# Optimization experiments

Measured on AMD Instinct MI355X. Metric: run time of the kernel, lower is better.

The kernel has to match this reference:

```python
import jax, jax.numpy as jnp
import numpy as np

N = 384      # max_nodes
H = 256      # layers[0] == layers[1] == layers[2]
Z = 128      # dim_z
ED = 128     # edge_dim
AH = ED // 2 # attention hidden

# complete directed graph: combinations (i<j) then reversed pairs
_i, _j = np.triu_indices(N, k=1)
_SRC = jnp.asarray(np.concatenate([_i, _j]), dtype=jnp.int32)  # edge_index[0]
_DST = jnp.asarray(np.concatenate([_j, _i]), dtype=jnp.int32)  # edge_index[1]


def setup_inputs() -> dict:
    key = jax.random.key(0)
    ks = jax.random.split(key, 16)
    def p(k, shape, fan_in):
        return jax.random.normal(k, shape, dtype=jnp.float32) * (1.0 / np.sqrt(fan_in))
    return {
        "z": jax.random.normal(ks[0], (1, Z), dtype=jnp.float32),
        # GRU (torch layout: W_ih [3H, Z], W_hh [3H, H]; gate order r, z, n)
        "gru_Wih": p(ks[1], (3 * H, Z), Z),
        "gru_Whh": p(ks[2], (3 * H, H), H),
        "gru_bih": jnp.zeros((3 * H,), jnp.float32),
        "gru_bhh": jnp.zeros((3 * H,), jnp.float32),
        # edge_generator MLP: 2H -> 4H -> ED
        "eg_W1": p(ks[3], (2 * H, 4 * H), 2 * H), "eg_b1": jnp.zeros((4 * H,), jnp.float32),
        "eg_W2": p(ks[4], (4 * H, ED), 4 * H),   "eg_b2": jnp.zeros((ED,), jnp.float32),
        # attention MLPs: (ED+H) -> ED//2 -> 1
        "att0_W1": p(ks[5], (ED + H, AH), ED + H), "att0_b1": jnp.zeros((AH,), jnp.float32),
        "att0_W2": p(ks[6], (AH, 1), AH),           "att0_b2": jnp.zeros((1,), jnp.float32),
        "att1_W1": p(ks[7], (ED + H, AH), ED + H), "att1_b1": jnp.zeros((AH,), jnp.float32),
        "att1_W2": p(ks[8], (AH, 1), AH),           "att1_b2": jnp.zeros((1,), jnp.float32),
        # EdgeConv output linears: H -> H
        "conv0_W": p(ks[9], (H, H), H),  "conv0_b": jnp.zeros((H,), jnp.float32),
        "conv1_W": p(ks[10], (H, H), H), "conv1_b": jnp.zeros((H,), jnp.float32),
    }


def _forward(z, gru_Wih, gru_Whh, gru_bih, gru_bhh,
             eg_W1, eg_b1, eg_W2, eg_b2,
             att0_W1, att0_b1, att0_W2, att0_b2,
             att1_W1, att1_b1, att1_W2, att1_b2,
             conv0_W, conv0_b, conv1_W, conv1_b):
    # --- GRU node generation: input is the same latent z at every step ---
    gi = z[0] @ gru_Wih.T + gru_bih            # [3H], constant per step
    gir, giz, gin = jnp.split(gi, 3)
    def step(h, _):
        gh = h @ gru_Whh.T + gru_bhh
        ghr, ghz, ghn = jnp.split(gh, 3)
        r = jax.nn.sigmoid(gir + ghr)
        u = jax.nn.sigmoid(giz + ghz)
        n = jnp.tanh(gin + r * ghn)
        h2 = (1.0 - u) * n + u * h
        return h2, h2
    _, nodes = jax.lax.scan(step, jnp.zeros((H,), z.dtype), None, length=N)  # [N, H]

    # --- edge features over the complete directed graph ---
    pairs = jnp.concatenate([nodes[_SRC], nodes[_DST]], axis=-1)            # [E, 2H]
    edges = jax.nn.relu(pairs @ eg_W1 + eg_b1) @ eg_W2 + eg_b2              # [E, ED]

    # --- EdgeConv: gather src, attention MLP gate, scatter-sum, linear ---
    def conv(x, aW1, ab1, aW2, ab2, W, b):
        xs = x[_SRC]                                                        # [E, H]
        a_in = jnp.concatenate([edges, xs], axis=-1)                        # [E, ED+H]
        att = jax.nn.sigmoid(jax.nn.relu(a_in @ aW1 + ab1) @ aW2 + ab2)     # [E, 1]
        agg = jax.ops.segment_sum(att * xs, _DST, num_segments=N)           # [N, H]
        return agg @ W + b

    x = jax.nn.relu(conv(nodes, att0_W1, att0_b1, att0_W2, att0_b2, conv0_W, conv0_b))
    x = conv(x, att1_W1, att1_b1, att1_W2, att1_b2, conv1_W, conv1_b)
    return jnp.sum(x, axis=0)                                               # [H]


def reference(z, gru_Wih, gru_Whh, gru_bih, gru_bhh,
              eg_W1, eg_b1, eg_W2, eg_b2,
              att0_W1, att0_b1, att0_W2, att0_b2,
              att1_W1, att1_b1, att1_W2, att1_b2,
              conv0_W, conv0_b, conv1_W, conv1_b):
    return _forward(z, gru_Wih, gru_Whh, gru_bih, gru_bhh,
                    eg_W1, eg_b1, eg_W2, eg_b2,
                    att0_W1, att0_b1, att0_W2, att0_b2,
                    att1_W1, att1_b1, att1_W2, att1_b2,
                    conv0_W, conv0_b, conv1_W, conv1_b)
```

## Files before the change

### kernel.cpp

```cpp
#include <hip/hip_runtime.h>
#include <hip/hip_fp16.h>
#include <cstdint>

#define DEV static __device__ __forceinline__

typedef _Float16 h2v __attribute__((ext_vector_type(2)));
typedef _Float16 half8 __attribute__((ext_vector_type(8)));
typedef float float4v __attribute__((ext_vector_type(4)));

union U32H2 { uint32_t u; _Float16 f[2]; };

DEV uint32_t pack_f2(float a, float b) {
    auto p = __builtin_amdgcn_cvt_pkrtz(a, b);
    return __builtin_bit_cast(uint32_t, p);
}

DEV half8 bc8(uint4 v) { return __builtin_bit_cast(half8, v); }

DEV float sigmoidf_(float x) { return 1.0f / (1.0f + __expf(-x)); }

DEV void gl_lds16(const void* gsrc, void* ldst) {
    __builtin_amdgcn_global_load_lds(
        (const __attribute__((address_space(1))) uint32_t*)gsrc,
        (__attribute__((address_space(3))) uint32_t*)ldst, 16, 0, 0);
}

DEV float pick4(float4v lo, float4v hi, int bsel, int r) {
    float v0 = bsel ? hi[0] : lo[0];
    float v1 = bsel ? hi[1] : lo[1];
    float v2 = bsel ? hi[2] : lo[2];
    float v3 = bsel ? hi[3] : lo[3];
    float x01 = (r & 1) ? v1 : v0;
    float x23 = (r & 1) ? v3 : v2;
    return (r & 2) ? x23 : x01;
}

static const size_t OFF_W16T  = 0;
static const size_t OFF_GI    = 98304;
static const size_t OFF_CC    = 99072;
static const size_t OFF_BF    = 99200;
static const size_t OFF_NODES = 164736;
static const size_t OFF_PF    = 263040;
static const size_t OFF_QF    = 459648;
static const size_t OFF_R0    = 656256;
static const size_t OFF_R1    = 680832;
static const size_t OFF_TT    = 705408;
static const size_t OFF_ATT0  = 10142592;
static const size_t OFF_ATT1  = 10290048;
static const size_t OFF_AGG   = 10437504;
static const size_t OFF_X0    = 10535808;
static const size_t OFF_CS    = 10634112;
static const size_t OFF_V     = 10634496;
static const size_t WS_TOTAL  = 10634752;

__global__ void k_prep_w16(const float* __restrict__ Whh, uint32_t* __restrict__ WL) {
    int o4 = blockIdx.x * 256 + threadIdx.x;
    int c = o4 >> 9, t = o4 & 511;
    int rt = c >> 3, kt = c & 7;
    int lane = t & 63, wv = t >> 6;
    int row = (rt >> 1) * 256 + wv * 32 + ((rt & 1) << 4) + (lane & 15);
    int k0 = kt*32 + (lane >> 4)*8;
    const float* src = Whh + row*256 + k0;
    uint4 o;
    o.x = pack_f2(src[0], src[1]);
    o.y = pack_f2(src[2], src[3]);
    o.z = pack_f2(src[4], src[5]);
    o.w = pack_f2(src[6], src[7]);
    ((uint4*)WL)[o4] = o;
}

__global__ void k_prep_gi(const float* __restrict__ z, const float* __restrict__ Wih,
                          const float* __restrict__ bih, const float* __restrict__ bhh,
                          float* __restrict__ gs) {
    int o = blockIdx.x * 256 + threadIdx.x;
    float acc = bih[o];
    if (o < 512) acc += bhh[o];
    for (int i = 0; i < 128; ++i) acc += Wih[o*128 + i] * z[i];
    gs[o] = acc;
}

__global__ void k_prep_cc(const float* __restrict__ eg_b2, const float* __restrict__ a0W1,
                          const float* __restrict__ a1W1, float* __restrict__ cc) {
    int t = threadIdx.x;
    const float* A = (t < 64) ? a0W1 : a1W1;
    int j = t & 63;
    float acc = 0.f;
    for (int i = 0; i < 128; ++i) acc += eg_b2[i] * A[i*64 + j];
    cc[t] = acc;
}

__global__ void k_prep_w2a(const float* __restrict__ eg_W2, const float* __restrict__ a0W1,
                           const float* __restrict__ a1W1, uint32_t* __restrict__ BF) {
    int idx = blockIdx.x * 256 + threadIdx.x;
    int k2 = idx >> 7, n = idx & 127;
    const float* A = (n < 64) ? (a0W1 + n) : (a1W1 + (n - 64));
    const float* w0 = eg_W2 + (2*k2) * 128;
    float a = 0.f, b = 0.f;
    for (int i = 0; i < 128; ++i) {
        float av = A[i*64];
        a += w0[i] * av;
        b += w0[128 + i] * av;
    }
    int kk = k2 >> 4, jgrp = (k2 >> 2) & 3, sub = k2 & 3;
    int lane = jgrp*16 + (n & 15), t = n >> 4;
    BF[((kk*8 + t)*64 + lane)*4 + sub] = pack_f2(a, b);
}

__global__ void __launch_bounds__(512, 2)
k_gru(const float* __restrict__ gs, const float* __restrict__ bhh,
      const uint32_t* __restrict__ WL, float* __restrict__ nodes) {
    int tid = threadIdx.x;
    int lane = tid & 63, wv = tid >> 6;
    int kq = lane >> 4, c = lane & 15;
    __shared__ __align__(16) _Float16 hh16[512];

    uint4 w[48];
    const uint4* wl4 = (const uint4*)WL;
    #pragma unroll
    for (int cc = 0; cc < 48; ++cc) w[cc] = wl4[cc*512 + tid];
    #pragma unroll
    for (int cc = 0; cc < 48; ++cc)
        asm volatile("" : "+a"(w[cc].x), "+a"(w[cc].y), "+a"(w[cc].z), "+a"(w[cc].w));

    const float L2E = 1.44269504088896f;
    int r = c & 3, bsel = (c >> 2) & 1;
    int i_loc = kq*4 + r + bsel*16;
    int gidx = wv*32 + i_loc;
    float pr = -L2E * gs[gidx];
    float pz = -L2E * gs[256 + gidx];
    float gin_l = gs[512 + gidx];
    float bn_l  = bhh[512 + gidx];
    float pn = -2.f * L2E * gin_l;
    bool active = (c < 8);

    float h = 0.f;
    if (tid < 256) ((uint32_t*)hh16)[tid] = 0u;
    __syncthreads();

    const float4v z4 = {0.f, 0.f, 0.f, 0.f};
    int par = 0;
    for (int t = 0; t < 384; ++t) {
        const _Float16* hb = hh16 + par*256 + kq*8;
        uint4 b[8];
        #pragma unroll
        for (int kt = 0; kt < 8; ++kt) b[kt] = *(const uint4*)(hb + kt*32);

        float4v d[6];
        #pragma unroll
        for (int rt = 0; rt < 6; ++rt)
            d[rt] = __builtin_amdgcn_mfma_f32_16x16x32_f16(bc8(w[rt*8]), bc8(b[0]), z4, 0, 0, 0);
        #pragma unroll
        for (int kt = 1; kt < 8; ++kt)
            #pragma unroll
            for (int rt = 0; rt < 6; ++rt)
                d[rt] = __builtin_amdgcn_mfma_f32_16x16x32_f16(bc8(w[rt*8 + kt]), bc8(b[kt]), d[rt], 0, 0, 0);

        float ghr = pick4(d[0], d[1], bsel, r);
        float ghz = pick4(d[2], d[3], bsel, r);
        float ghn = pick4(d[4], d[5], bsel, r);

        float er = __builtin_amdgcn_exp2f(__builtin_fmaf(ghr, -L2E, pr));
        float rg = __builtin_amdgcn_rcpf(1.f + er);
        float eu = __builtin_amdgcn_exp2f(__builtin_fmaf(ghz, -L2E, pz));
        float u  = __builtin_amdgcn_rcpf(1.f + eu);
        float tm = ghn + bn_l;
        float q  = __builtin_fmaf(rg * tm, -2.f * L2E, pn);
        float e2 = __builtin_amdgcn_exp2f(q);
        float nn = __builtin_fmaf(2.f, __builtin_amdgcn_rcpf(1.f + e2), -1.f);
        h = nn + u * (h - nn);

        if (active) {
            hh16[(par ^ 1)*256 + gidx] = (_Float16)h;
            nodes[t*256 + gidx] = h;
        }
        asm volatile("s_waitcnt lgkmcnt(0)" ::: "memory");
        __builtin_amdgcn_sched_barrier(0);
        __builtin_amdgcn_s_barrier();
        __builtin_amdgcn_sched_barrier(0);
        par ^= 1;
    }
}

__global__ void k_pq(const float* __restrict__ nodes, const float* __restrict__ eg_W1,
                     const float* __restrict__ eg_b1, const float* __restrict__ a0W1,
                     const float* __restrict__ a0b1, const float* __restrict__ cc,
                     uint32_t* __restrict__ PF, uint32_t* __restrict__ QF,
                     float* __restrict__ R0) {
    int tid = threadIdx.x;
    int s0 = blockIdx.x * 4;
    __shared__ float ns[4][256];
    #pragma unroll
    for (int q = 0; q < 4; ++q) ns[q][tid] = nodes[(s0+q)*256 + tid];
    __syncthreads();

    int k0 = tid * 4;
    float acc[4][4];
    #pragma unroll
    for (int q = 0; q < 4; ++q) { acc[q][0]=0;acc[q][1]=0;acc[q][2]=0;acc[q][3]=0; }
    for (int i = 0; i < 256; ++i) {
        float4 wv = *(const float4*)&eg_W1[i*1024 + k0];
        #pragma unroll
        for (int q = 0; q < 4; ++q) {
            float nv = ns[q][i];
            acc[q][0] += nv*wv.x; acc[q][1] += nv*wv.y;
            acc[q][2] += nv*wv.z; acc[q][3] += nv*wv.w;
        }
    }
    float4 bv = *(const float4*)&eg_b1[k0];
    {
        int kk = k0 >> 5;
        int lgrp = ((k0 >> 3) & 3) * 16;
        int sub = (k0 & 7) >> 1;
        #pragma unroll
        for (int q = 0; q < 4; ++q) {
            int s = s0 + q, g = s >> 4, srow = s & 15;
            uint2 pw;
            pw.x = pack_f2(acc[q][0] + bv.x, acc[q][1] + bv.y);
            pw.y = pack_f2(acc[q][2] + bv.z, acc[q][3] + bv.w);
            *(uint2*)(PF + (((g*32 + kk)*64 + lgrp + srow) << 2) + sub) = pw;
        }
    }

    #pragma unroll
    for (int q = 0; q < 4; ++q) { acc[q][0]=0;acc[q][1]=0;acc[q][2]=0;acc[q][3]=0; }
    for (int i = 0; i < 256; ++i) {
        float4 wv = *(const float4*)&eg_W1[(256+i)*1024 + k0];
        #pragma unroll
        for (int q = 0; q < 4; ++q) {
            float nv = ns[q][i];
            acc[q][0] += nv*wv.x; acc[q][1] += nv*wv.y;
            acc[q][2] += nv*wv.z; acc[q][3] += nv*wv.w;
        }
    }
    #pragma unroll
    for (int q = 0; q < 4; ++q) {
        uint2 pw;
        pw.x = pack_f2(acc[q][0], acc[q][1]);
        pw.y = pack_f2(acc[q][2], acc[q][3]);
        ((uint2*)QF)[(s0+q)*256 + tid] = pw;
    }

    int srow = tid >> 6, j = tid & 63;
    float racc = a0b1[j] + cc[j];
    for (int i = 0; i < 256; ++i) racc += ns[srow][i] * a0W1[(128+i)*64 + j];
    R0[(s0+srow)*64 + j] = racc;
}

__global__ void __launch_bounds__(256, 2)
k_phaseA_mfma(const uint32_t* __restrict__ PF, const uint32_t* __restrict__ QF,
              const uint32_t* __restrict__ BF, uint32_t* __restrict__ TT) {
    __shared__ __align__(16) char smem[69632];
    uint4* Qs4 = (uint4*)smem;
    uint4* Ps4 = (uint4*)(smem + 32768);
    uint4* Bs4 = (uint4*)(smem + 36864);

    int tid = threadIdx.x;
    int lane = tid & 63, wv = tid >> 6;
    int g = blockIdx.x, d0 = blockIdx.y * 16;

    {
        const char* src = (const char*)(QF + (size_t)d0 * 512);
        for (int off = wv*1024 + lane*16; off < 32768; off += 4096)
            gl_lds16(src + off, (char*)Qs4 + off);
    }

    float4v acc[4][8];
    #pragma unroll
    for (int t = 0; t < 4; ++t)
        #pragma unroll
        for (int n = 0; n < 8; ++n) acc[t][n] = 0.f;

    for (int c = 0; c < 8; ++c) {
        __syncthreads();
        {
            const char* psrc = (const char*)(PF + (size_t)(g*32 + c*4) * 256);
            for (int off = wv*1024 + lane*16; off < 4096; off += 4096)
                gl_lds16(psrc + off, (char*)Ps4 + off);
            const char* bsrc = (const char*)(BF + (size_t)c * 8192);
            for (int off = wv*1024 + lane*16; off < 32768; off += 4096)
                gl_lds16(bsrc + off, (char*)Bs4 + off);
        }
        __syncthreads();

        #pragma unroll
        for (int kkl = 0; kkl < 4; ++kkl) {
            int kkg = c*4 + kkl;
            half8 b[8];
            #pragma unroll
            for (int n = 0; n < 8; ++n) b[n] = bc8(Bs4[(kkl*8 + n)*64 + lane]);
            half8 p8 = bc8(Ps4[kkl*64 + lane]);
            #pragma unroll
            for (int t = 0; t < 4; ++t) {
                half8 q8 = bc8(Qs4[(wv*4 + t)*128 + kkg*4 + (lane >> 4)]);
                half8 x = p8 + q8;
                half8 z = 0;
                x = __builtin_elementwise_max(x, z);
                #pragma unroll
                for (int n = 0; n < 8; ++n)
                    acc[t][n] = __builtin_amdgcn_mfma_f32_16x16x32_f16(x, b[n], acc[t][n], 0, 0, 0);
            }
        }
    }

    _Float16* epi = (_Float16*)(smem + 36864);
    int cn = lane & 15, rhi = (lane >> 4) * 4;
    for (int half = 0; half < 2; ++half) {
        __syncthreads();
        #pragma unroll
        for (int t = 0; t < 4; ++t) {
            int dl = wv*4 + t;
            #pragma unroll
            for (int n = 0; n < 4; ++n) {
                int j = n*16 + cn;
                float4v v = acc[t][half*4 + n];
                #pragma unroll
                for (int r = 0; r < 4; ++r)
                    epi[((rhi + r)*16 + dl)*64 + j] = (_Float16)v[r];
            }
        }
        __syncthreads();
        int srow = tid >> 4, dl = tid & 15;
        const uint4* src = (const uint4*)(epi + tid*64);
        uint4* dst = (uint4*)(TT + ((size_t)((g*16 + srow)*384 + d0 + dl))*64 + half*32);
        #pragma unroll
        for (int q = 0; q < 8; ++q) dst[q] = src[q];
    }
}

__global__ void k_att(const uint32_t* __restrict__ TT, const float* __restrict__ R,
                      const float* __restrict__ w2, const float* __restrict__ b2,
                      int off, float* __restrict__ ATT) {
    int p = blockIdx.x * 256 + threadIdx.x;
    int s = p / 384, d = p - s * 384;
    __shared__ float w2s[64];
    if (threadIdx.x < 64) w2s[threadIdx.x] = w2[threadIdx.x];
    __syncthreads();
    const uint4* tp = (const uint4*)(TT + (size_t)p*64 + off);
    const float* rp = R + s*64;
    float logit = b2[0];
    #pragma unroll
    for (int m = 0; m < 8; ++m) {
        uint4 tv = tp[m];
        uint32_t us[4] = {tv.x, tv.y, tv.z, tv.w};
        #pragma unroll
        for (int q = 0; q < 4; ++q) {
            U32H2 c; c.u = us[q];
            int j = m*8 + q*2;
            float h0 = fmaxf((float)c.f[0] + rp[j],   0.f);
            float h1 = fmaxf((float)c.f[1] + rp[j+1], 0.f);
            logit += h0*w2s[j] + h1*w2s[j+1];
        }
    }
    float a = 1.f / (1.f + __expf(-logit));
    ATT[p] = (s == d) ? 0.f : a;
}

__global__ void __launch_bounds__(256)
k_agg(const float* __restrict__ ATT, const float* __restrict__ X,
      float* __restrict__ AGG) {
    int tid = threadIdx.x;
    int d0 = blockIdx.x * 16;
    __shared__ float att_s[16][17];
    float acc[16];
    #pragma unroll
    for (int dl = 0; dl < 16; ++dl) acc[dl] = 0.f;

    for (int s0 = 0; s0 < 384; s0 += 16) {
        __syncthreads();
        {
            int row = tid >> 4, col = tid & 15;
            att_s[row][col] = ATT[(s0 + row)*384 + d0 + col];
        }
        __syncthreads();
        #pragma unroll 4
        for (int ss = 0; ss < 16; ++ss) {
            float x = X[(s0 + ss)*256 + tid];
            #pragma unroll
            for (int dl = 0; dl < 16; ++dl) acc[dl] += att_s[ss][dl] * x;
        }
    }
    #pragma unroll
    for (int dl = 0; dl < 16; ++dl)
        AGG[(d0 + dl)*256 + tid] = acc[dl];
}

__global__ void k_x0r1(const float* __restrict__ AGG, const float* __restrict__ W,
                       const float* __restrict__ b, const float* __restrict__ a1W1,
                       const float* __restrict__ a1b1, const float* __restrict__ cc,
                       float* __restrict__ X0, float* __restrict__ R1) {
    int d = blockIdx.x, tid = threadIdx.x;
    __shared__ float ag[256];
    __shared__ float xs[256];
    ag[tid] = AGG[d*256 + tid];
    __syncthreads();
    float acc = b[tid];
    for (int i = 0; i < 256; ++i) acc += ag[i] * W[i*256 + tid];
    acc = fmaxf(acc, 0.f);
    X0[d*256 + tid] = acc;
    xs[tid] = acc;
    __syncthreads();
    if (tid < 64) {
        float r = a1b1[tid] + cc[64 + tid];
        for (int i = 0; i < 256; ++i) r += xs[i] * a1W1[(128+i)*64 + tid];
        R1[d*64 + tid] = r;
    }
}

__global__ void k_colsum(const float* __restrict__ ATT, float* __restrict__ CS) {
    int s = blockIdx.x, t = threadIdx.x;
    float acc = 0.f;
    for (int d = t; d < 384; d += 64) acc += ATT[s*384 + d];
    for (int o = 32; o > 0; o >>= 1) acc += __shfl_down(acc, o, 64);
    if (t == 0) CS[s] = acc;
}

__global__ void k_v(const float* __restrict__ CS, const float* __restrict__ X0,
                    float* __restrict__ V) {
    int tid = threadIdx.x;
    __shared__ float cs[384];
    for (int q = tid; q < 384; q += 256) cs[q] = CS[q];
    __syncthreads();
    float acc = 0.f;
    for (int s = 0; s < 384; s += 4) {
        acc += cs[s]*X0[s*256 + tid] + cs[s+1]*X0[(s+1)*256 + tid]
             + cs[s+2]*X0[(s+2)*256 + tid] + cs[s+3]*X0[(s+3)*256 + tid];
    }
    V[tid] = acc;
}

__global__ void k_out(const float* __restrict__ V, const float* __restrict__ W,
                      const float* __restrict__ b, float* __restrict__ out) {
    int tid = threadIdx.x;
    __shared__ float vs[256];
    vs[tid] = V[tid];
    __syncthreads();
    float acc = 384.f * b[tid];
    for (int i = 0; i < 256; ++i) acc += vs[i] * W[i*256 + tid];
    out[tid] = acc;
}

extern "C" void kernel_launch(void* const* d_in, const int* in_sizes, int n_in,
                              void* d_out, int out_size, void* d_ws, size_t ws_size,
                              hipStream_t stream) {
    if (ws_size < WS_TOTAL * sizeof(uint32_t)) return;

    const float* z    = (const float*)d_in[0];
    const float* Wih  = (const float*)d_in[1];
    const float* Whh  = (const float*)d_in[2];
    const float* bih  = (const float*)d_in[3];
    const float* bhh  = (const float*)d_in[4];
    const float* egW1 = (const float*)d_in[5];
    const float* egb1 = (const float*)d_in[6];
    const float* egW2 = (const float*)d_in[7];
    const float* egb2 = (const float*)d_in[8];
    const float* a0W1 = (const float*)d_in[9];
    const float* a0b1 = (const float*)d_in[10];
    const float* a0W2 = (const float*)d_in[11];
    const float* a0b2 = (const float*)d_in[12];
    const float* a1W1 = (const float*)d_in[13];
    const float* a1b1 = (const float*)d_in[14];
    const float* a1W2 = (const float*)d_in[15];
    const float* a1b2 = (const float*)d_in[16];
    const float* c0W  = (const float*)d_in[17];
    const float* c0b  = (const float*)d_in[18];
    const float* c1W  = (const float*)d_in[19];
    const float* c1b  = (const float*)d_in[20];

    uint32_t* ws   = (uint32_t*)d_ws;
    uint32_t* WL   = ws + OFF_W16T;
    float*    gi   = (float*)(ws + OFF_GI);
    float*    cc   = (float*)(ws + OFF_CC);
    uint32_t* BF   = ws + OFF_BF;
    float*    nodes= (float*)(ws + OFF_NODES);
    uint32_t* PF   = ws + OFF_PF;
    uint32_t* QF   = ws + OFF_QF;
    float*    R0   = (float*)(ws + OFF_R0);
    float*    R1   = (float*)(ws + OFF_R1);
    uint32_t* TT   = ws + OFF_TT;
    float*    ATT0 = (float*)(ws + OFF_ATT0);
    float*    ATT1 = (float*)(ws + OFF_ATT1);
    float*    AGG  = (float*)(ws + OFF_AGG);
    float*    X0   = (float*)(ws + OFF_X0);
    float*    CS   = (float*)(ws + OFF_CS);
    float*    V    = (float*)(ws + OFF_V);
    float*    out  = (float*)d_out;

    hipLaunchKernelGGL(k_prep_w16,    dim3(96),  dim3(256), 0, stream, Whh, WL);
    hipLaunchKernelGGL(k_prep_gi,     dim3(3),   dim3(256), 0, stream, z, Wih, bih, bhh, gi);
    hipLaunchKernelGGL(k_prep_cc,     dim3(1),   dim3(128), 0, stream, egb2, a0W1, a1W1, cc);
    hipLaunchKernelGGL(k_prep_w2a,    dim3(256), dim3(256), 0, stream, egW2, a0W1, a1W1, BF);
    hipLaunchKernelGGL(k_gru,         dim3(1),   dim3(512), 0, stream, gi, bhh, WL, nodes);
    hipLaunchKernelGGL(k_pq,          dim3(96),  dim3(256), 0, stream, nodes, egW1, egb1, a0W1, a0b1, cc, PF, QF, R0);
    hipLaunchKernelGGL(k_phaseA_mfma, dim3(24, 24), dim3(256), 0, stream, PF, QF, BF, TT);
    hipLaunchKernelGGL(k_att,         dim3(576), dim3(256), 0, stream, TT, R0, a0W2, a0b2, 0,  ATT0);
    hipLaunchKernelGGL(k_agg,         dim3(24),  dim3(256), 0, stream, ATT0, nodes, AGG);
    hipLaunchKernelGGL(k_x0r1,        dim3(384), dim3(256), 0, stream, AGG, c0W, c0b, a1W1, a1b1, cc, X0, R1);
    hipLaunchKernelGGL(k_att,         dim3(576), dim3(256), 0, stream, TT, R1, a1W2, a1b2, 32, ATT1);
    hipLaunchKernelGGL(k_colsum,      dim3(384), dim3(64),  0, stream, ATT1, CS);
    hipLaunchKernelGGL(k_v,           dim3(1),   dim3(256), 0, stream, CS, X0, V);
    hipLaunchKernelGGL(k_out,         dim3(1),   dim3(256), 0, stream, V, c1W, c1b, out);
}
```

Measured before the change: 704.8 us.

## Merge prep kernels, double-buffer phase-A staging, fuse colsum/out, reorder GRU gates

The four weight-prep kernels become one launch, and the colsum, v and out kernels fold into an atomic column sum inside the second attention kernel plus a single k_vout kernel. Phase A now double-buffers the P/B tiles in half-chunks so the next tile loads while the current one is multiplied. The GRU step computes the reset-gate MFMAs first so its sigmoid can overlap the remaining gate MFMAs, and k_att caches the R rows in shared memory. The goal is fewer launches and less exposed latency; the atomics add a memset and make the float summation order nondeterministic.

```diff
diff --git a/kernel.cpp b/kernel.cpp
--- a/kernel.cpp
+++ b/kernel.cpp
@@ -53,57 +53,58 @@
 static const size_t OFF_V     = 10634496;
 static const size_t WS_TOTAL  = 10634752;
 
-__global__ void k_prep_w16(const float* __restrict__ Whh, uint32_t* __restrict__ WL) {
-    int o4 = blockIdx.x * 256 + threadIdx.x;
-    int c = o4 >> 9, t = o4 & 511;
-    int rt = c >> 3, kt = c & 7;
-    int lane = t & 63, wv = t >> 6;
-    int row = (rt >> 1) * 256 + wv * 32 + ((rt & 1) << 4) + (lane & 15);
-    int k0 = kt*32 + (lane >> 4)*8;
-    const float* src = Whh + row*256 + k0;
-    uint4 o;
-    o.x = pack_f2(src[0], src[1]);
-    o.y = pack_f2(src[2], src[3]);
-    o.z = pack_f2(src[4], src[5]);
-    o.w = pack_f2(src[6], src[7]);
-    ((uint4*)WL)[o4] = o;
-}
-
-__global__ void k_prep_gi(const float* __restrict__ z, const float* __restrict__ Wih,
-                          const float* __restrict__ bih, const float* __restrict__ bhh,
-                          float* __restrict__ gs) {
-    int o = blockIdx.x * 256 + threadIdx.x;
-    float acc = bih[o];
-    if (o < 512) acc += bhh[o];
-    for (int i = 0; i < 128; ++i) acc += Wih[o*128 + i] * z[i];
-    gs[o] = acc;
-}
-
-__global__ void k_prep_cc(const float* __restrict__ eg_b2, const float* __restrict__ a0W1,
-                          const float* __restrict__ a1W1, float* __restrict__ cc) {
-    int t = threadIdx.x;
-    const float* A = (t < 64) ? a0W1 : a1W1;
-    int j = t & 63;
-    float acc = 0.f;
-    for (int i = 0; i < 128; ++i) acc += eg_b2[i] * A[i*64 + j];
-    cc[t] = acc;
-}
-
-__global__ void k_prep_w2a(const float* __restrict__ eg_W2, const float* __restrict__ a0W1,
-                           const float* __restrict__ a1W1, uint32_t* __restrict__ BF) {
-    int idx = blockIdx.x * 256 + threadIdx.x;
-    int k2 = idx >> 7, n = idx & 127;
-    const float* A = (n < 64) ? (a0W1 + n) : (a1W1 + (n - 64));
-    const float* w0 = eg_W2 + (2*k2) * 128;
-    float a = 0.f, b = 0.f;
-    for (int i = 0; i < 128; ++i) {
-        float av = A[i*64];
-        a += w0[i] * av;
-        b += w0[128 + i] * av;
-    }
-    int kk = k2 >> 4, jgrp = (k2 >> 2) & 3, sub = k2 & 3;
-    int lane = jgrp*16 + (n & 15), t = n >> 4;
-    BF[((kk*8 + t)*64 + lane)*4 + sub] = pack_f2(a, b);
+__global__ void k_prep_all(const float* __restrict__ Whh, uint32_t* __restrict__ WL,
+                           const float* __restrict__ z, const float* __restrict__ Wih,
+                           const float* __restrict__ bih, const float* __restrict__ bhh,
+                           float* __restrict__ gs,
+                           const float* __restrict__ egb2, const float* __restrict__ a0W1,
+                           const float* __restrict__ a1W1, float* __restrict__ cc,
+                           const float* __restrict__ egW2, uint32_t* __restrict__ BF) {
+    int bb = blockIdx.x;
+    if (bb < 96) {
+        int o4 = bb * 256 + threadIdx.x;
+        int c = o4 >> 9, t = o4 & 511;
+        int rt = c >> 3, kt = c & 7;
+        int lane = t & 63, wv = t >> 6;
+        int row = (rt >> 1) * 256 + wv * 32 + ((rt & 1) << 4) + (lane & 15);
+        int k0 = kt*32 + (lane >> 4)*8;
+        const float* src = Whh + row*256 + k0;
+        uint4 o;
+        o.x = pack_f2(src[0], src[1]);
+        o.y = pack_f2(src[2], src[3]);
+        o.z = pack_f2(src[4], src[5]);
+        o.w = pack_f2(src[6], src[7]);
+        ((uint4*)WL)[o4] = o;
+    } else if (bb < 99) {
+        int o = (bb - 96) * 256 + threadIdx.x;
+        float acc = bih[o];
+        if (o < 512) acc += bhh[o];
+        for (int i = 0; i < 128; ++i) acc += Wih[o*128 + i] * z[i];
+        gs[o] = acc;
+    } else if (bb == 99) {
+        int t = threadIdx.x;
+        if (t < 128) {
+            const float* A = (t < 64) ? a0W1 : a1W1;
+            int j = t & 63;
+            float acc = 0.f;
+            for (int i = 0; i < 128; ++i) acc += egb2[i] * A[i*64 + j];
+            cc[t] = acc;
+        }
+    } else {
+        int idx = (bb - 100) * 256 + threadIdx.x;
+        int k2 = idx >> 7, n = idx & 127;
+        const float* A = (n < 64) ? (a0W1 + n) : (a1W1 + (n - 64));
+        const float* w0 = egW2 + (2*k2) * 128;
+        float a = 0.f, b = 0.f;
+        for (int i = 0; i < 128; ++i) {
+            float av = A[i*64];
+            a += w0[i] * av;
+            b += w0[128 + i] * av;
+        }
+        int kk = k2 >> 4, jgrp = (k2 >> 2) & 3, sub = k2 & 3;
+        int lane = jgrp*16 + (n & 15), t = n >> 4;
+        BF[((kk*8 + t)*64 + lane)*4 + sub] = pack_f2(a, b);
+    }
 }
 
 __global__ void __launch_bounds__(512, 2)
@@ -145,22 +146,32 @@
         #pragma unroll
         for (int kt = 0; kt < 8; ++kt) b[kt] = *(const uint4*)(hb + kt*32);
 
-        float4v d[6];
-        #pragma unroll
-        for (int rt = 0; rt < 6; ++rt)
-            d[rt] = __builtin_amdgcn_mfma_f32_16x16x32_f16(bc8(w[rt*8]), bc8(b[0]), z4, 0, 0, 0);
-        #pragma unroll
-        for (int kt = 1; kt < 8; ++kt)
-            #pragma unroll
-            for (int rt = 0; rt < 6; ++rt)
-                d[rt] = __builtin_amdgcn_mfma_f32_16x16x32_f16(bc8(w[rt*8 + kt]), bc8(b[kt]), d[rt], 0, 0, 0);
-
-        float ghr = pick4(d[0], d[1], bsel, r);
-        float ghz = pick4(d[2], d[3], bsel, r);
-        float ghn = pick4(d[4], d[5], bsel, r);
-
+        float4v d0, d1, d2, d3, d4, d5;
+        d0 = __builtin_amdgcn_mfma_f32_16x16x32_f16(bc8(w[0]),  bc8(b[0]), z4, 0, 0, 0);
+        d1 = __builtin_amdgcn_mfma_f32_16x16x32_f16(bc8(w[8]),  bc8(b[0]), z4, 0, 0, 0);
+        #pragma unroll
+        for (int kt = 1; kt < 8; ++kt) {
+            d0 = __builtin_amdgcn_mfma_f32_16x16x32_f16(bc8(w[kt]),    bc8(b[kt]), d0, 0, 0, 0);
+            d1 = __builtin_amdgcn_mfma_f32_16x16x32_f16(bc8(w[8+kt]),  bc8(b[kt]), d1, 0, 0, 0);
+        }
+        float ghr = pick4(d0, d1, bsel, r);
         float er = __builtin_amdgcn_exp2f(__builtin_fmaf(ghr, -L2E, pr));
         float rg = __builtin_amdgcn_rcpf(1.f + er);
+
+        d2 = __builtin_amdgcn_mfma_f32_16x16x32_f16(bc8(w[16]), bc8(b[0]), z4, 0, 0, 0);
+        d3 = __builtin_amdgcn_mfma_f32_16x16x32_f16(bc8(w[24]), bc8(b[0]), z4, 0, 0, 0);
+        d4 = __builtin_amdgcn_mfma_f32_16x16x32_f16(bc8(w[32]), bc8(b[0]), z4, 0, 0, 0);
+        d5 = __builtin_amdgcn_mfma_f32_16x16x32_f16(bc8(w[40]), bc8(b[0]), z4, 0, 0, 0);
+        #pragma unroll
+        for (int kt = 1; kt < 8; ++kt) {
+            d2 = __builtin_amdgcn_mfma_f32_16x16x32_f16(bc8(w[16+kt]), bc8(b[kt]), d2, 0, 0, 0);
+            d3 = __builtin_amdgcn_mfma_f32_16x16x32_f16(bc8(w[24+kt]), bc8(b[kt]), d3, 0, 0, 0);
+            d4 = __builtin_amdgcn_mfma_f32_16x16x32_f16(bc8(w[32+kt]), bc8(b[kt]), d4, 0, 0, 0);
+            d5 = __builtin_amdgcn_mfma_f32_16x16x32_f16(bc8(w[40+kt]), bc8(b[kt]), d5, 0, 0, 0);
+        }
+
+        float ghz = pick4(d2, d3, bsel, r);
+        float ghn = pick4(d4, d5, bsel, r);
         float eu = __builtin_amdgcn_exp2f(__builtin_fmaf(ghz, -L2E, pz));
         float u  = __builtin_amdgcn_rcpf(1.f + eu);
         float tm = ghn + bn_l;
@@ -246,13 +257,22 @@
     R0[(s0+srow)*64 + j] = racc;
 }
 
+DEV void stageA(const uint32_t* __restrict__ PF, const uint32_t* __restrict__ BF,
+                int g, int hc, char* buf, int tid) {
+    const char* psrc = (const char*)(PF + ((size_t)g*32 + (size_t)hc*2) * 256);
+    if (tid < 128) gl_lds16(psrc + tid*16, buf + tid*16);
+    const char* bsrc = (const char*)(BF + (size_t)hc * 4096);
+    #pragma unroll
+    for (int i = 0; i < 4; ++i)
+        gl_lds16(bsrc + tid*16 + i*4096, buf + 2048 + tid*16 + i*4096);
+}
+
 __global__ void __launch_bounds__(256, 2)
 k_phaseA_mfma(const uint32_t* __restrict__ PF, const uint32_t* __restrict__ QF,
               const uint32_t* __restrict__ BF, uint32_t* __restrict__ TT) {
     __shared__ __align__(16) char smem[69632];
     uint4* Qs4 = (uint4*)smem;
-    uint4* Ps4 = (uint4*)(smem + 32768);
-    uint4* Bs4 = (uint4*)(smem + 36864);
+    char* bufbase = smem + 32768;
 
     int tid = threadIdx.x;
     int lane = tid & 63, wv = tid >> 6;
@@ -260,9 +280,16 @@
 
     {
         const char* src = (const char*)(QF + (size_t)d0 * 512);
-        for (int off = wv*1024 + lane*16; off < 32768; off += 4096)
-            gl_lds16(src + off, (char*)Qs4 + off);
-    }
+        int off = tid * 16;
+        #pragma unroll
+        for (int i = 0; i < 8; ++i)
+            gl_lds16(src + off + i*4096, (char*)Qs4 + off + i*4096);
+    }
+    stageA(PF, BF, g, 0, bufbase, tid);
+    asm volatile("s_waitcnt vmcnt(0)" ::: "memory");
+    __builtin_amdgcn_sched_barrier(0);
+    __builtin_amdgcn_s_barrier();
+    __builtin_amdgcn_sched_barrier(0);
 
     float4v acc[4][8];
     #pragma unroll
@@ -270,39 +297,38 @@
         #pragma unroll
         for (int n = 0; n < 8; ++n) acc[t][n] = 0.f;
 
-    for (int c = 0; c < 8; ++c) {
-        __syncthreads();
-        {
-            const char* psrc = (const char*)(PF + (size_t)(g*32 + c*4) * 256);
-            for (int off = wv*1024 + lane*16; off < 4096; off += 4096)
-                gl_lds16(psrc + off, (char*)Ps4 + off);
-            const char* bsrc = (const char*)(BF + (size_t)c * 8192);
-            for (int off = wv*1024 + lane*16; off < 32768; off += 4096)
-                gl_lds16(bsrc + off, (char*)Bs4 + off);
-        }
-        __syncthreads();
-
-        #pragma unroll
-        for (int kkl = 0; kkl < 4; ++kkl) {
-            int kkg = c*4 + kkl;
+    for (int hc = 0; hc < 16; ++hc) {
+        char* cur = bufbase + (hc & 1) * 18432;
+        char* nxt = bufbase + ((hc + 1) & 1) * 18432;
+        if (hc < 15) stageA(PF, BF, g, hc + 1, nxt, tid);
+
+        uint4* Ph = (uint4*)cur;
+        uint4* Bh = (uint4*)(cur + 2048);
+        #pragma unroll
+        for (int kkl = 0; kkl < 2; ++kkl) {
+            int kkg = hc*2 + kkl;
             half8 b[8];
             #pragma unroll
-            for (int n = 0; n < 8; ++n) b[n] = bc8(Bs4[(kkl*8 + n)*64 + lane]);
-            half8 p8 = bc8(Ps4[kkl*64 + lane]);
+            for (int n = 0; n < 8; ++n) b[n] = bc8(Bh[(kkl*8 + n)*64 + lane]);
+            half8 p8 = bc8(Ph[kkl*64 + lane]);
             #pragma unroll
             for (int t = 0; t < 4; ++t) {
                 half8 q8 = bc8(Qs4[(wv*4 + t)*128 + kkg*4 + (lane >> 4)]);
                 half8 x = p8 + q8;
-                half8 z = 0;
-                x = __builtin_elementwise_max(x, z);
+                half8 zz = 0;
+                x = __builtin_elementwise_max(x, zz);
                 #pragma unroll
                 for (int n = 0; n < 8; ++n)
                     acc[t][n] = __builtin_amdgcn_mfma_f32_16x16x32_f16(x, b[n], acc[t][n], 0, 0, 0);
             }
         }
-    }
-
-    _Float16* epi = (_Float16*)(smem + 36864);
+        asm volatile("s_waitcnt vmcnt(0)" ::: "memory");
+        __builtin_amdgcn_sched_barrier(0);
+        __builtin_amdgcn_s_barrier();
+        __builtin_amdgcn_sched_barrier(0);
+    }
+
+    _Float16* epi = (_Float16*)(smem + 32768);
     int cn = lane & 15, rhi = (lane >> 4) * 4;
     for (int half = 0; half < 2; ++half) {
         __syncthreads();
@@ -329,14 +355,22 @@
 
 __global__ void k_att(const uint32_t* __restrict__ TT, const float* __restrict__ R,
                       const float* __restrict__ w2, const float* __restrict__ b2,
-                      int off, float* __restrict__ ATT) {
-    int p = blockIdx.x * 256 + threadIdx.x;
+                      int off, float* __restrict__ ATT, float* __restrict__ CS) {
+    int tid = threadIdx.x;
+    int p = blockIdx.x * 256 + tid;
     int s = p / 384, d = p - s * 384;
+    int sa = (blockIdx.x * 256) / 384;
     __shared__ float w2s[64];
-    if (threadIdx.x < 64) w2s[threadIdx.x] = w2[threadIdx.x];
+    __shared__ float rs[2][64];
+    if (tid < 64) w2s[tid] = w2[tid];
+    else if (tid < 128) rs[0][tid - 64] = R[sa*64 + (tid - 64)];
+    else if (tid < 192) {
+        int sb = sa + 1;
+        rs[1][tid - 128] = (sb < 384) ? R[sb*64 + (tid - 128)] : 0.f;
+    }
     __syncthreads();
     const uint4* tp = (const uint4*)(TT + (size_t)p*64 + off);
-    const float* rp = R + s*64;
+    const float* rp = (s == sa) ? rs[0] : rs[1];
     float logit = b2[0];
     #pragma unroll
     for (int m = 0; m < 8; ++m) {
@@ -352,7 +386,23 @@
         }
     }
     float a = 1.f / (1.f + __expf(-logit));
-    ATT[p] = (s == d) ? 0.f : a;
+    float a_eff = (s == d) ? 0.f : a;
+    ATT[p] = a_eff;
+
+    if (CS) {
+        float va = (s == sa) ? a_eff : 0.f;
+        float vb = (s != sa) ? a_eff : 0.f;
+        #pragma unroll
+        for (int o = 32; o > 0; o >>= 1) {
+            va += __shfl_down(va, o, 64);
+            vb += __shfl_down(vb, o, 64);
+        }
+        if ((tid & 63) == 0) {
+            atomicAdd(&CS[sa], va);
+            int sb = sa + 1;
+            if (sb < 384) atomicAdd(&CS[sb], vb);
+        }
+    }
 }
 
 __global__ void __launch_bounds__(256)
@@ -406,18 +456,12 @@
     }
 }
 
-__global__ void k_colsum(const float* __restrict__ ATT, float* __restrict__ CS) {
-    int s = blockIdx.x, t = threadIdx.x;
-    float acc = 0.f;
-    for (int d = t; d < 384; d += 64) acc += ATT[s*384 + d];
-    for (int o = 32; o > 0; o >>= 1) acc += __shfl_down(acc, o, 64);
-    if (t == 0) CS[s] = acc;
-}
-
-__global__ void k_v(const float* __restrict__ CS, const float* __restrict__ X0,
-                    float* __restrict__ V) {
+__global__ void k_vout(const float* __restrict__ CS, const float* __restrict__ X0,
+                       const float* __restrict__ W, const float* __restrict__ b,
+                       float* __restrict__ out) {
     int tid = threadIdx.x;
     __shared__ float cs[384];
+    __shared__ float vs[256];
     for (int q = tid; q < 384; q += 256) cs[q] = CS[q];
     __syncthreads();
     float acc = 0.f;
@@ -425,18 +469,11 @@
         acc += cs[s]*X0[s*256 + tid] + cs[s+1]*X0[(s+1)*256 + tid]
              + cs[s+2]*X0[(s+2)*256 + tid] + cs[s+3]*X0[(s+3)*256 + tid];
     }
-    V[tid] = acc;
-}
-
-__global__ void k_out(const float* __restrict__ V, const float* __restrict__ W,
-                      const float* __restrict__ b, float* __restrict__ out) {
-    int tid = threadIdx.x;
-    __shared__ float vs[256];
-    vs[tid] = V[tid];
-    __syncthreads();
-    float acc = 384.f * b[tid];
-    for (int i = 0; i < 256; ++i) acc += vs[i] * W[i*256 + tid];
-    out[tid] = acc;
+    vs[tid] = acc;
+    __syncthreads();
+    float o = 384.f * b[tid];
+    for (int i = 0; i < 256; ++i) o += vs[i] * W[i*256 + tid];
+    out[tid] = o;
 }
 
 extern "C" void kernel_launch(void* const* d_in, const int* in_sizes, int n_in,
@@ -482,21 +519,17 @@
     float*    AGG  = (float*)(ws + OFF_AGG);
     float*    X0   = (float*)(ws + OFF_X0);
     float*    CS   = (float*)(ws + OFF_CS);
-    float*    V    = (float*)(ws + OFF_V);
     float*    out  = (float*)d_out;
 
-    hipLaunchKernelGGL(k_prep_w16,    dim3(96),  dim3(256), 0, stream, Whh, WL);
-    hipLaunchKernelGGL(k_prep_gi,     dim3(3),   dim3(256), 0, stream, z, Wih, bih, bhh, gi);
-    hipLaunchKernelGGL(k_prep_cc,     dim3(1),   dim3(128), 0, stream, egb2, a0W1, a1W1, cc);
-    hipLaunchKernelGGL(k_prep_w2a,    dim3(256), dim3(256), 0, stream, egW2, a0W1, a1W1, BF);
+    hipMemsetAsync(CS, 0, 384 * sizeof(float), stream);
+    hipLaunchKernelGGL(k_prep_all,    dim3(356), dim3(256), 0, stream,
+                       Whh, WL, z, Wih, bih, bhh, gi, egb2, a0W1, a1W1, cc, egW2, BF);
     hipLaunchKernelGGL(k_gru,         dim3(1),   dim3(512), 0, stream, gi, bhh, WL, nodes);
     hipLaunchKernelGGL(k_pq,          dim3(96),  dim3(256), 0, stream, nodes, egW1, egb1, a0W1, a0b1, cc, PF, QF, R0);
     hipLaunchKernelGGL(k_phaseA_mfma, dim3(24, 24), dim3(256), 0, stream, PF, QF, BF, TT);
-    hipLaunchKernelGGL(k_att,         dim3(576), dim3(256), 0, stream, TT, R0, a0W2, a0b2, 0,  ATT0);
+    hipLaunchKernelGGL(k_att,         dim3(576), dim3(256), 0, stream, TT, R0, a0W2, a0b2, 0,  ATT0, (float*)nullptr);
     hipLaunchKernelGGL(k_agg,         dim3(24),  dim3(256), 0, stream, ATT0, nodes, AGG);
     hipLaunchKernelGGL(k_x0r1,        dim3(384), dim3(256), 0, stream, AGG, c0W, c0b, a1W1, a1b1, cc, X0, R1);
-    hipLaunchKernelGGL(k_att,         dim3(576), dim3(256), 0, stream, TT, R1, a1W2, a1b2, 32, ATT1);
-    hipLaunchKernelGGL(k_colsum,      dim3(384), dim3(64),  0, stream, ATT1, CS);
-    hipLaunchKernelGGL(k_v,           dim3(1),   dim3(256), 0, stream, CS, X0, V);
-    hipLaunchKernelGGL(k_out,         dim3(1),   dim3(256), 0, stream, V, c1W, c1b, out);
-}
+    hipLaunchKernelGGL(k_att,         dim3(576), dim3(256), 0, stream, TT, R1, a1W2, a1b2, 32, ATT1, CS);
+    hipLaunchKernelGGL(k_vout,        dim3(1),   dim3(256), 0, stream, CS, X0, c1W, c1b, out);
+}
```

After: 699.5 us. Within noise of the previous version (-0.8%).
